# Optimization experiments

Hardware: AMD Instinct MI355X
Metric: run time of the kernel (lower is better)

The kernel has to match this reference:

```python
import jax, jax.numpy as jnp
import numpy as np

N_ROWS = 8388608          # multiple of 4, as required by the chunked linear
N_SEGMENTS = 4096


def setup_inputs() -> dict:
    key = jax.random.key(0)
    kx, ks = jax.random.split(key)
    x = jax.random.normal(kx, (N_ROWS, 4), dtype=jnp.float32)
    # monotone segment boundaries: 0 = slices[0] <= ... <= slices[-1] = N_ROWS
    interior = jnp.sort(jax.random.randint(ks, (N_SEGMENTS - 1,), 1, N_ROWS, dtype=jnp.int32))
    slices = jnp.concatenate([jnp.zeros((1,), jnp.int32), interior,
                              jnp.full((1,), N_ROWS, jnp.int32)])
    # fixed weight from the original module: arange(16).reshape(4, 4)
    W = jnp.arange(16, dtype=jnp.float32).reshape(4, 4)
    return {"x": x, "slices": slices, "W": W}


def reference(x, slices, W):
    # Chunked 4-row linear == plain matmul with the same weight (nn.Linear: y = x @ W.T)
    y = x @ W.T                                           # [N, 4]
    n = y.shape[0]
    # segment id of each row: number of boundaries <= row index, minus 1
    seg = jnp.searchsorted(slices, jnp.arange(n, dtype=slices.dtype), side="right") - 1
    seg = jnp.clip(seg, 0, N_SEGMENTS - 1)
    # per-segment sum of |y| over all elements (rows and features)
    seg_abs = jax.ops.segment_sum(jnp.abs(y).sum(-1), seg, num_segments=N_SEGMENTS)  # [S]
    return y / seg_abs[seg][:, None]
```

## Files before the change

### kernel.cpp

```cpp
#include <hip/hip_runtime.h>


#define NSEG  4096
#define BLK   256
#define RPT   16
#define BATCH 8
#define CHUNK (BLK * RPT)

typedef float v4 __attribute__((ext_vector_type(4)));

__device__ __forceinline__ float absrow(v4 v, const float* w) {
    float y0 = fabsf(v.x * w[0]  + v.y * w[1]  + v.z * w[2]  + v.w * w[3]);
    float y1 = fabsf(v.x * w[4]  + v.y * w[5]  + v.z * w[6]  + v.w * w[7]);
    float y2 = fabsf(v.x * w[8]  + v.y * w[9]  + v.z * w[10] + v.w * w[11]);
    float y3 = fabsf(v.x * w[12] + v.y * w[13] + v.z * w[14] + v.w * w[15]);
    return (y0 + y1) + (y2 + y3);
}

__global__ __launch_bounds__(BLK) void seg_pass1(
    const v4* __restrict__ x, const int* __restrict__ slices,
    const float* __restrict__ W, float* __restrict__ seg_abs, int n)
{
    __shared__ int   sl[NSEG + 1];
    __shared__ float hist[NSEG];
#pragma unroll
    for (int i = threadIdx.x; i < NSEG + 1; i += BLK) sl[i] = slices[i];
#pragma unroll
    for (int i = threadIdx.x; i < NSEG; i += BLK) hist[i] = 0.0f;

    float w[16];
#pragma unroll
    for (int i = 0; i < 16; ++i) w[i] = W[i];
    __syncthreads();

    const int base = blockIdx.x * CHUNK + threadIdx.x;

    int lo = 0, hi = NSEG;
    {
        int r0 = (base < n) ? base : (n - 1);
        while (hi - lo > 1) { int mid = (lo + hi) >> 1; if (sl[mid] <= r0) lo = mid; else hi = mid; }
    }
    int seg = lo;
    float acc = 0.0f;

    const bool full = (base + (RPT - 1) * BLK) < n;
    if (full) {
#pragma unroll
        for (int b = 0; b < RPT / BATCH; ++b) {
            v4 d[BATCH];
#pragma unroll
            for (int j = 0; j < BATCH; ++j)
                d[j] = x[base + (b * BATCH + j) * BLK];
#pragma unroll
            for (int j = 0; j < BATCH; ++j) {
                int r = base + (b * BATCH + j) * BLK;
                int s = seg;
                while (s < NSEG - 1 && sl[s + 1] <= r) ++s;
                if (s != seg) { atomicAdd(&hist[seg], acc); acc = 0.0f; seg = s; }
                acc += absrow(d[j], w);
            }
        }
    } else {
        for (int it = 0; it < RPT; ++it) {
            int r = base + it * BLK;
            if (r < n) {
                int s = seg;
                while (s < NSEG - 1 && sl[s + 1] <= r) ++s;
                if (s != seg) { atomicAdd(&hist[seg], acc); acc = 0.0f; seg = s; }
                acc += absrow(x[r], w);
            }
        }
    }
    if (acc != 0.0f) atomicAdd(&hist[seg], acc);
    __syncthreads();

#pragma unroll
    for (int i = threadIdx.x; i < NSEG; i += BLK) {
        float h = hist[i];
        if (h != 0.0f) atomicAdd(&seg_abs[i], h);
    }
}

__global__ __launch_bounds__(BLK) void seg_pass2(
    const v4* __restrict__ x, const int* __restrict__ slices,
    const float* __restrict__ W, const float* __restrict__ seg_abs,
    v4* __restrict__ out, int n)
{
    __shared__ int sl[NSEG + 1];
#pragma unroll
    for (int i = threadIdx.x; i < NSEG + 1; i += BLK) sl[i] = slices[i];

    float w[16];
#pragma unroll
    for (int i = 0; i < 16; ++i) w[i] = W[i];
    __syncthreads();

    const int base = blockIdx.x * CHUNK + threadIdx.x;

    int lo = 0, hi = NSEG;
    {
        int r0 = (base < n) ? base : (n - 1);
        while (hi - lo > 1) { int mid = (lo + hi) >> 1; if (sl[mid] <= r0) lo = mid; else hi = mid; }
    }
    int seg = lo;
    float inv = 1.0f / seg_abs[seg];

    const bool full = (base + (RPT - 1) * BLK) < n;
    if (full) {
#pragma unroll
        for (int b = 0; b < RPT / BATCH; ++b) {
            v4 d[BATCH];
#pragma unroll
            for (int j = 0; j < BATCH; ++j)
                d[j] = x[base + (b * BATCH + j) * BLK];
#pragma unroll
            for (int j = 0; j < BATCH; ++j) {
                int r = base + (b * BATCH + j) * BLK;
                int s = seg;
                while (s < NSEG - 1 && sl[s + 1] <= r) ++s;
                if (s != seg) { seg = s; inv = 1.0f / seg_abs[seg]; }
                v4 v = d[j], o;
                o.x = (v.x * w[0]  + v.y * w[1]  + v.z * w[2]  + v.w * w[3])  * inv;
                o.y = (v.x * w[4]  + v.y * w[5]  + v.z * w[6]  + v.w * w[7])  * inv;
                o.z = (v.x * w[8]  + v.y * w[9]  + v.z * w[10] + v.w * w[11]) * inv;
                o.w = (v.x * w[12] + v.y * w[13] + v.z * w[14] + v.w * w[15]) * inv;
                __builtin_nontemporal_store(o, &out[r]);
            }
        }
    } else {
        for (int it = 0; it < RPT; ++it) {
            int r = base + it * BLK;
            if (r < n) {
                int s = seg;
                while (s < NSEG - 1 && sl[s + 1] <= r) ++s;
                if (s != seg) { seg = s; inv = 1.0f / seg_abs[seg]; }
                v4 v = x[r], o;
                o.x = (v.x * w[0]  + v.y * w[1]  + v.z * w[2]  + v.w * w[3])  * inv;
                o.y = (v.x * w[4]  + v.y * w[5]  + v.z * w[6]  + v.w * w[7])  * inv;
                o.z = (v.x * w[8]  + v.y * w[9]  + v.z * w[10] + v.w * w[11]) * inv;
                o.w = (v.x * w[12] + v.y * w[13] + v.z * w[14] + v.w * w[15]) * inv;
                __builtin_nontemporal_store(o, &out[r]);
            }
        }
    }
}

extern "C" void kernel_launch(void* const* d_in, const int* in_sizes, int n_in,
                              void* d_out, int out_size, void* d_ws, size_t ws_size,
                              hipStream_t stream) {
    const v4*   x      = (const v4*)d_in[0];
    const int*  slices = (const int*)d_in[1];
    const float* W     = (const float*)d_in[2];
    float*      seg_abs = (float*)d_ws;
    v4*         out    = (v4*)d_out;
    int n = in_sizes[0] / 4;

    hipMemsetAsync(d_ws, 0, NSEG * sizeof(float), stream);

    int nblocks = (n + CHUNK - 1) / CHUNK;
    seg_pass1<<<nblocks, BLK, 0, stream>>>(x, slices, W, seg_abs, n);
    seg_pass2<<<nblocks, BLK, 0, stream>>>(x, slices, W, seg_abs, out, n);
}
```

Baseline: 265.5 us.

## Fuse both passes into one persistent cooperative kernel with grid sync

Replaces the memset plus two kernel launches with a single cooperative persistent kernel. Each block keeps its shared-memory histogram across all the chunks it processes and flushes it to global memory after a grid-wide sync, then a second sync precedes the normalisation pass. This cuts launch overhead and the number of global atomics, but pass 2 still rereads x, and grid-wide syncs plus lower occupancy from shared memory use are added. The old two-pass path is kept only as a fallback and loses its batched loads.

```diff
diff --git a/kernel.cpp b/kernel.cpp
--- a/kernel.cpp
+++ b/kernel.cpp
@@ -1,4 +1,7 @@
 #include <hip/hip_runtime.h>
+#include <hip/hip_cooperative_groups.h>
+
+namespace cg = cooperative_groups;
 
 
 #define NSEG  4096
@@ -6,6 +9,7 @@
 #define RPT   16
 #define BATCH 8
 #define CHUNK (BLK * RPT)
+#define NCU   256
 
 typedef float v4 __attribute__((ext_vector_type(4)));
 
@@ -17,6 +21,127 @@
     return (y0 + y1) + (y2 + y3);
 }
 
+__global__ __launch_bounds__(BLK, 4) void seg_fused(
+    const v4* __restrict__ x, const int* __restrict__ slices,
+    const float* __restrict__ W, float* __restrict__ seg_abs,
+    v4* __restrict__ out, int n, int nchunks)
+{
+    __shared__ int   sl[NSEG];
+    __shared__ float hist[NSEG];
+#pragma unroll
+    for (int i = threadIdx.x; i < NSEG; i += BLK) { sl[i] = slices[i]; hist[i] = 0.0f; }
+
+    for (int i = blockIdx.x * BLK + threadIdx.x; i < NSEG; i += gridDim.x * BLK)
+        atomicExch(&seg_abs[i], 0.0f);
+
+    float w[16];
+#pragma unroll
+    for (int i = 0; i < 16; ++i) w[i] = W[i];
+    __syncthreads();
+
+    for (int c = blockIdx.x; c < nchunks; c += gridDim.x) {
+        const int base = c * CHUNK + threadIdx.x;
+        int lo = 0, hi = NSEG;
+        {
+            int r0 = (base < n) ? base : (n - 1);
+            while (hi - lo > 1) { int mid = (lo + hi) >> 1; if (sl[mid] <= r0) lo = mid; else hi = mid; }
+        }
+        int seg = lo;
+        float acc = 0.0f;
+
+        const bool full = (base + (RPT - 1) * BLK) < n;
+        if (full) {
+#pragma unroll
+            for (int b = 0; b < RPT / BATCH; ++b) {
+                v4 d[BATCH];
+#pragma unroll
+                for (int j = 0; j < BATCH; ++j)
+                    d[j] = x[base + (b * BATCH + j) * BLK];
+#pragma unroll
+                for (int j = 0; j < BATCH; ++j) {
+                    int r = base + (b * BATCH + j) * BLK;
+                    int s = seg;
+                    while (s < NSEG - 1 && sl[s + 1] <= r) ++s;
+                    if (s != seg) { atomicAdd(&hist[seg], acc); acc = 0.0f; seg = s; }
+                    acc += absrow(d[j], w);
+                }
+            }
+        } else {
+            for (int it = 0; it < RPT; ++it) {
+                int r = base + it * BLK;
+                if (r < n) {
+                    int s = seg;
+                    while (s < NSEG - 1 && sl[s + 1] <= r) ++s;
+                    if (s != seg) { atomicAdd(&hist[seg], acc); acc = 0.0f; seg = s; }
+                    acc += absrow(x[r], w);
+                }
+            }
+        }
+        if (acc != 0.0f) atomicAdd(&hist[seg], acc);
+    }
+    __syncthreads();
+
+    cg::grid_group grid = cg::this_grid();
+    grid.sync();
+
+#pragma unroll
+    for (int i = threadIdx.x; i < NSEG; i += BLK) {
+        float h = hist[i];
+        if (h != 0.0f) atomicAdd(&seg_abs[i], h);
+    }
+    grid.sync();
+
+    for (int c = blockIdx.x; c < nchunks; c += gridDim.x) {
+        const int base = c * CHUNK + threadIdx.x;
+        int lo = 0, hi = NSEG;
+        {
+            int r0 = (base < n) ? base : (n - 1);
+            while (hi - lo > 1) { int mid = (lo + hi) >> 1; if (sl[mid] <= r0) lo = mid; else hi = mid; }
+        }
+        int seg = lo;
+        float inv = 1.0f / seg_abs[seg];
+
+        const bool full = (base + (RPT - 1) * BLK) < n;
+        if (full) {
+#pragma unroll
+            for (int b = 0; b < RPT / BATCH; ++b) {
+                v4 d[BATCH];
+#pragma unroll
+                for (int j = 0; j < BATCH; ++j)
+                    d[j] = x[base + (b * BATCH + j) * BLK];
+#pragma unroll
+                for (int j = 0; j < BATCH; ++j) {
+                    int r = base + (b * BATCH + j) * BLK;
+                    int s = seg;
+                    while (s < NSEG - 1 && sl[s + 1] <= r) ++s;
+                    if (s != seg) { seg = s; inv = 1.0f / seg_abs[seg]; }
+                    v4 v = d[j], o;
+                    o.x = (v.x * w[0]  + v.y * w[1]  + v.z * w[2]  + v.w * w[3])  * inv;
+                    o.y = (v.x * w[4]  + v.y * w[5]  + v.z * w[6]  + v.w * w[7])  * inv;
+                    o.z = (v.x * w[8]  + v.y * w[9]  + v.z * w[10] + v.w * w[11]) * inv;
+                    o.w = (v.x * w[12] + v.y * w[13] + v.z * w[14] + v.w * w[15]) * inv;
+                    __builtin_nontemporal_store(o, &out[r]);
+                }
+            }
+        } else {
+            for (int it = 0; it < RPT; ++it) {
+                int r = base + it * BLK;
+                if (r < n) {
+                    int s = seg;
+                    while (s < NSEG - 1 && sl[s + 1] <= r) ++s;
+                    if (s != seg) { seg = s; inv = 1.0f / seg_abs[seg]; }
+                    v4 v = x[r], o;
+                    o.x = (v.x * w[0]  + v.y * w[1]  + v.z * w[2]  + v.w * w[3])  * inv;
+                    o.y = (v.x * w[4]  + v.y * w[5]  + v.z * w[6]  + v.w * w[7])  * inv;
+                    o.z = (v.x * w[8]  + v.y * w[9]  + v.z * w[10] + v.w * w[11]) * inv;
+                    o.w = (v.x * w[12] + v.y * w[13] + v.z * w[14] + v.w * w[15]) * inv;
+                    __builtin_nontemporal_store(o, &out[r]);
+                }
+            }
+        }
+    }
+}
+
 __global__ __launch_bounds__(BLK) void seg_pass1(
     const v4* __restrict__ x, const int* __restrict__ slices,
     const float* __restrict__ W, float* __restrict__ seg_abs, int n)
@@ -27,14 +152,12 @@
     for (int i = threadIdx.x; i < NSEG + 1; i += BLK) sl[i] = slices[i];
 #pragma unroll
     for (int i = threadIdx.x; i < NSEG; i += BLK) hist[i] = 0.0f;
-
     float w[16];
 #pragma unroll
     for (int i = 0; i < 16; ++i) w[i] = W[i];
     __syncthreads();
 
     const int base = blockIdx.x * CHUNK + threadIdx.x;
-
     int lo = 0, hi = NSEG;
     {
         int r0 = (base < n) ? base : (n - 1);
@@ -42,38 +165,17 @@
     }
     int seg = lo;
     float acc = 0.0f;
-
-    const bool full = (base + (RPT - 1) * BLK) < n;
-    if (full) {
-#pragma unroll
-        for (int b = 0; b < RPT / BATCH; ++b) {
-            v4 d[BATCH];
-#pragma unroll
-            for (int j = 0; j < BATCH; ++j)
-                d[j] = x[base + (b * BATCH + j) * BLK];
-#pragma unroll
-            for (int j = 0; j < BATCH; ++j) {
-                int r = base + (b * BATCH + j) * BLK;
-                int s = seg;
-                while (s < NSEG - 1 && sl[s + 1] <= r) ++s;
-                if (s != seg) { atomicAdd(&hist[seg], acc); acc = 0.0f; seg = s; }
-                acc += absrow(d[j], w);
-            }
-        }
-    } else {
-        for (int it = 0; it < RPT; ++it) {
-            int r = base + it * BLK;
-            if (r < n) {
-                int s = seg;
-                while (s < NSEG - 1 && sl[s + 1] <= r) ++s;
-                if (s != seg) { atomicAdd(&hist[seg], acc); acc = 0.0f; seg = s; }
-                acc += absrow(x[r], w);
-            }
+    for (int it = 0; it < RPT; ++it) {
+        int r = base + it * BLK;
+        if (r < n) {
+            int s = seg;
+            while (s < NSEG - 1 && sl[s + 1] <= r) ++s;
+            if (s != seg) { atomicAdd(&hist[seg], acc); acc = 0.0f; seg = s; }
+            acc += absrow(x[r], w);
         }
     }
     if (acc != 0.0f) atomicAdd(&hist[seg], acc);
     __syncthreads();
-
 #pragma unroll
     for (int i = threadIdx.x; i < NSEG; i += BLK) {
         float h = hist[i];
@@ -89,14 +191,12 @@
     __shared__ int sl[NSEG + 1];
 #pragma unroll
     for (int i = threadIdx.x; i < NSEG + 1; i += BLK) sl[i] = slices[i];
-
     float w[16];
 #pragma unroll
     for (int i = 0; i < 16; ++i) w[i] = W[i];
     __syncthreads();
 
     const int base = blockIdx.x * CHUNK + threadIdx.x;
-
     int lo = 0, hi = NSEG;
     {
         int r0 = (base < n) ? base : (n - 1);
@@ -104,43 +204,18 @@
     }
     int seg = lo;
     float inv = 1.0f / seg_abs[seg];
-
-    const bool full = (base + (RPT - 1) * BLK) < n;
-    if (full) {
-#pragma unroll
-        for (int b = 0; b < RPT / BATCH; ++b) {
-            v4 d[BATCH];
-#pragma unroll
-            for (int j = 0; j < BATCH; ++j)
-                d[j] = x[base + (b * BATCH + j) * BLK];
-#pragma unroll
-            for (int j = 0; j < BATCH; ++j) {
-                int r = base + (b * BATCH + j) * BLK;
-                int s = seg;
-                while (s < NSEG - 1 && sl[s + 1] <= r) ++s;
-                if (s != seg) { seg = s; inv = 1.0f / seg_abs[seg]; }
-                v4 v = d[j], o;
-                o.x = (v.x * w[0]  + v.y * w[1]  + v.z * w[2]  + v.w * w[3])  * inv;
-                o.y = (v.x * w[4]  + v.y * w[5]  + v.z * w[6]  + v.w * w[7])  * inv;
-                o.z = (v.x * w[8]  + v.y * w[9]  + v.z * w[10] + v.w * w[11]) * inv;
-                o.w = (v.x * w[12] + v.y * w[13] + v.z * w[14] + v.w * w[15]) * inv;
-                __builtin_nontemporal_store(o, &out[r]);
-            }
-        }
-    } else {
-        for (int it = 0; it < RPT; ++it) {
-            int r = base + it * BLK;
-            if (r < n) {
-                int s = seg;
-                while (s < NSEG - 1 && sl[s + 1] <= r) ++s;
-                if (s != seg) { seg = s; inv = 1.0f / seg_abs[seg]; }
-                v4 v = x[r], o;
-                o.x = (v.x * w[0]  + v.y * w[1]  + v.z * w[2]  + v.w * w[3])  * inv;
-                o.y = (v.x * w[4]  + v.y * w[5]  + v.z * w[6]  + v.w * w[7])  * inv;
-                o.z = (v.x * w[8]  + v.y * w[9]  + v.z * w[10] + v.w * w[11]) * inv;
-                o.w = (v.x * w[12] + v.y * w[13] + v.z * w[14] + v.w * w[15]) * inv;
-                __builtin_nontemporal_store(o, &out[r]);
-            }
+    for (int it = 0; it < RPT; ++it) {
+        int r = base + it * BLK;
+        if (r < n) {
+            int s = seg;
+            while (s < NSEG - 1 && sl[s + 1] <= r) ++s;
+            if (s != seg) { seg = s; inv = 1.0f / seg_abs[seg]; }
+            v4 v = x[r], o;
+            o.x = (v.x * w[0]  + v.y * w[1]  + v.z * w[2]  + v.w * w[3])  * inv;
+            o.y = (v.x * w[4]  + v.y * w[5]  + v.z * w[6]  + v.w * w[7])  * inv;
+            o.z = (v.x * w[8]  + v.y * w[9]  + v.z * w[10] + v.w * w[11]) * inv;
+            o.w = (v.x * w[12] + v.y * w[13] + v.z * w[14] + v.w * w[15]) * inv;
+            __builtin_nontemporal_store(o, &out[r]);
         }
     }
 }
@@ -148,16 +223,31 @@
 extern "C" void kernel_launch(void* const* d_in, const int* in_sizes, int n_in,
                               void* d_out, int out_size, void* d_ws, size_t ws_size,
                               hipStream_t stream) {
-    const v4*   x      = (const v4*)d_in[0];
-    const int*  slices = (const int*)d_in[1];
-    const float* W     = (const float*)d_in[2];
-    float*      seg_abs = (float*)d_ws;
-    v4*         out    = (v4*)d_out;
-    int n = in_sizes[0] / 4;
-
-    hipMemsetAsync(d_ws, 0, NSEG * sizeof(float), stream);
-
-    int nblocks = (n + CHUNK - 1) / CHUNK;
-    seg_pass1<<<nblocks, BLK, 0, stream>>>(x, slices, W, seg_abs, n);
-    seg_pass2<<<nblocks, BLK, 0, stream>>>(x, slices, W, seg_abs, out, n);
-}
+    const v4*    x       = (const v4*)d_in[0];
+    const int*   slices  = (const int*)d_in[1];
+    const float* W       = (const float*)d_in[2];
+    float*       seg_abs = (float*)d_ws;
+    v4*          out     = (v4*)d_out;
+    int n       = in_sizes[0] / 4;
+    int nchunks = (n + CHUNK - 1) / CHUNK;
+
+    static int maxb = 0;
+    if (maxb == 0) {
+        if (hipOccupancyMaxActiveBlocksPerMultiprocessor(&maxb, seg_fused, BLK, 0)
+                != hipSuccess || maxb < 1)
+            maxb = 1;
+    }
+    int grid = nchunks < maxb * NCU ? nchunks : maxb * NCU;
+
+    void* args[] = { (void*)&x, (void*)&slices, (void*)&W, (void*)&seg_abs,
+                     (void*)&out, (void*)&n, (void*)&nchunks };
+    hipError_t err = hipLaunchCooperativeKernel((const void*)seg_fused,
+                                                dim3(grid), dim3(BLK),
+                                                args, 0, stream);
+    if (err != hipSuccess) {
+        hipMemsetAsync(d_ws, 0, NSEG * sizeof(float), stream);
+        int nblocks = (n + CHUNK - 1) / CHUNK;
+        seg_pass1<<<nblocks, BLK, 0, stream>>>(x, slices, W, seg_abs, n);
+        seg_pass2<<<nblocks, BLK, 0, stream>>>(x, slices, W, seg_abs, out, n);
+    }
+}
```

Result: slower. 491.7 us (+85.2%).

## Drop per-block shared copy of slices and full histogram; track next boundary from global

Applied to the files above, without the earlier changes.

Removes the per-block staging of all 4097 slice boundaries and the 4096-entry shared histogram in both passes. Boundaries are now read directly from global (cached) memory, with a running next-boundary register replacing the linear scan. Pass 1 keeps only a 64-entry windowed shared histogram relative to the block's first segment and falls back to global atomics beyond it. RPT is doubled so each block handles more rows, amortising setup. This cuts per-block prologue and epilogue work and LDS use, at the cost of dependent global loads in the binary search and possible global atomics.

```diff
diff --git a/kernel.cpp b/kernel.cpp
--- a/kernel.cpp
+++ b/kernel.cpp
@@ -3,9 +3,10 @@
 
 #define NSEG  4096
 #define BLK   256
-#define RPT   16
+#define RPT   32
 #define BATCH 8
 #define CHUNK (BLK * RPT)
+#define WSZ   64
 
 typedef float v4 __attribute__((ext_vector_type(4)));
 
@@ -17,31 +18,38 @@
     return (y0 + y1) + (y2 + y3);
 }
 
+__device__ __forceinline__ void flush_seg(float acc, int seg, int s0,
+                                          float* hist, float* __restrict__ seg_abs) {
+    if (acc == 0.0f) return;
+    int d = seg - s0;
+    if (d < WSZ) atomicAdd(&hist[d], acc);
+    else         atomicAdd(&seg_abs[seg], acc);
+}
+
 __global__ __launch_bounds__(BLK) void seg_pass1(
     const v4* __restrict__ x, const int* __restrict__ slices,
     const float* __restrict__ W, float* __restrict__ seg_abs, int n)
 {
-    __shared__ int   sl[NSEG + 1];
-    __shared__ float hist[NSEG];
-#pragma unroll
-    for (int i = threadIdx.x; i < NSEG + 1; i += BLK) sl[i] = slices[i];
-#pragma unroll
-    for (int i = threadIdx.x; i < NSEG; i += BLK) hist[i] = 0.0f;
+    __shared__ float hist[WSZ];
+    __shared__ int s0_sh;
+    if (threadIdx.x < WSZ) hist[threadIdx.x] = 0.0f;
 
     float w[16];
 #pragma unroll
     for (int i = 0; i < 16; ++i) w[i] = W[i];
-    __syncthreads();
 
     const int base = blockIdx.x * CHUNK + threadIdx.x;
 
+    int r0 = (base < n) ? base : (n - 1);
     int lo = 0, hi = NSEG;
-    {
-        int r0 = (base < n) ? base : (n - 1);
-        while (hi - lo > 1) { int mid = (lo + hi) >> 1; if (sl[mid] <= r0) lo = mid; else hi = mid; }
-    }
+    while (hi - lo > 1) { int mid = (lo + hi) >> 1; if (slices[mid] <= r0) lo = mid; else hi = mid; }
     int seg = lo;
-    float acc = 0.0f;
+    if (threadIdx.x == 0) s0_sh = seg;
+    __syncthreads();
+    const int s0 = s0_sh;
+
+    int   nextb = slices[seg + 1];
+    float acc   = 0.0f;
 
     const bool full = (base + (RPT - 1) * BLK) < n;
     if (full) {
@@ -54,9 +62,11 @@
 #pragma unroll
             for (int j = 0; j < BATCH; ++j) {
                 int r = base + (b * BATCH + j) * BLK;
-                int s = seg;
-                while (s < NSEG - 1 && sl[s + 1] <= r) ++s;
-                if (s != seg) { atomicAdd(&hist[seg], acc); acc = 0.0f; seg = s; }
+                if (r >= nextb) {
+                    flush_seg(acc, seg, s0, hist, seg_abs);
+                    acc = 0.0f;
+                    do { ++seg; nextb = slices[seg + 1]; } while (r >= nextb);
+                }
                 acc += absrow(d[j], w);
             }
         }
@@ -64,20 +74,21 @@
         for (int it = 0; it < RPT; ++it) {
             int r = base + it * BLK;
             if (r < n) {
-                int s = seg;
-                while (s < NSEG - 1 && sl[s + 1] <= r) ++s;
-                if (s != seg) { atomicAdd(&hist[seg], acc); acc = 0.0f; seg = s; }
+                if (r >= nextb) {
+                    flush_seg(acc, seg, s0, hist, seg_abs);
+                    acc = 0.0f;
+                    do { ++seg; nextb = slices[seg + 1]; } while (r >= nextb);
+                }
                 acc += absrow(x[r], w);
             }
         }
     }
-    if (acc != 0.0f) atomicAdd(&hist[seg], acc);
+    flush_seg(acc, seg, s0, hist, seg_abs);
     __syncthreads();
 
-#pragma unroll
-    for (int i = threadIdx.x; i < NSEG; i += BLK) {
-        float h = hist[i];
-        if (h != 0.0f) atomicAdd(&seg_abs[i], h);
+    if (threadIdx.x < WSZ) {
+        float h = hist[threadIdx.x];
+        if (h != 0.0f) atomicAdd(&seg_abs[s0 + threadIdx.x], h);
     }
 }
 
@@ -86,24 +97,19 @@
     const float* __restrict__ W, const float* __restrict__ seg_abs,
     v4* __restrict__ out, int n)
 {
-    __shared__ int sl[NSEG + 1];
-#pragma unroll
-    for (int i = threadIdx.x; i < NSEG + 1; i += BLK) sl[i] = slices[i];
-
     float w[16];
 #pragma unroll
     for (int i = 0; i < 16; ++i) w[i] = W[i];
-    __syncthreads();
 
     const int base = blockIdx.x * CHUNK + threadIdx.x;
 
+    int r0 = (base < n) ? base : (n - 1);
     int lo = 0, hi = NSEG;
-    {
-        int r0 = (base < n) ? base : (n - 1);
-        while (hi - lo > 1) { int mid = (lo + hi) >> 1; if (sl[mid] <= r0) lo = mid; else hi = mid; }
-    }
+    while (hi - lo > 1) { int mid = (lo + hi) >> 1; if (slices[mid] <= r0) lo = mid; else hi = mid; }
     int seg = lo;
-    float inv = 1.0f / seg_abs[seg];
+
+    int   nextb = slices[seg + 1];
+    float inv   = 1.0f / seg_abs[seg];
 
     const bool full = (base + (RPT - 1) * BLK) < n;
     if (full) {
@@ -116,9 +122,10 @@
 #pragma unroll
             for (int j = 0; j < BATCH; ++j) {
                 int r = base + (b * BATCH + j) * BLK;
-                int s = seg;
-                while (s < NSEG - 1 && sl[s + 1] <= r) ++s;
-                if (s != seg) { seg = s; inv = 1.0f / seg_abs[seg]; }
+                if (r >= nextb) {
+                    do { ++seg; nextb = slices[seg + 1]; } while (r >= nextb);
+                    inv = 1.0f / seg_abs[seg];
+                }
                 v4 v = d[j], o;
                 o.x = (v.x * w[0]  + v.y * w[1]  + v.z * w[2]  + v.w * w[3])  * inv;
                 o.y = (v.x * w[4]  + v.y * w[5]  + v.z * w[6]  + v.w * w[7])  * inv;
@@ -131,9 +138,10 @@
         for (int it = 0; it < RPT; ++it) {
             int r = base + it * BLK;
             if (r < n) {
-                int s = seg;
-                while (s < NSEG - 1 && sl[s + 1] <= r) ++s;
-                if (s != seg) { seg = s; inv = 1.0f / seg_abs[seg]; }
+                if (r >= nextb) {
+                    do { ++seg; nextb = slices[seg + 1]; } while (r >= nextb);
+                    inv = 1.0f / seg_abs[seg];
+                }
                 v4 v = x[r], o;
                 o.x = (v.x * w[0]  + v.y * w[1]  + v.z * w[2]  + v.w * w[3])  * inv;
                 o.y = (v.x * w[4]  + v.y * w[5]  + v.z * w[6]  + v.w * w[7])  * inv;
@@ -148,11 +156,11 @@
 extern "C" void kernel_launch(void* const* d_in, const int* in_sizes, int n_in,
                               void* d_out, int out_size, void* d_ws, size_t ws_size,
                               hipStream_t stream) {
-    const v4*   x      = (const v4*)d_in[0];
-    const int*  slices = (const int*)d_in[1];
-    const float* W     = (const float*)d_in[2];
-    float*      seg_abs = (float*)d_ws;
-    v4*         out    = (v4*)d_out;
+    const v4*    x       = (const v4*)d_in[0];
+    const int*   slices  = (const int*)d_in[1];
+    const float* W       = (const float*)d_in[2];
+    float*       seg_abs = (float*)d_ws;
+    v4*          out     = (v4*)d_out;
     int n = in_sizes[0] / 4;
 
     hipMemsetAsync(d_ws, 0, NSEG * sizeof(float), stream);
```

After: 261.1 us. Within noise of the previous version (-1.7%).
